# Performance work log

Hardware: AMD Instinct MI355X
Metric: run time of the kernel (lower is better)

## Reference

```python
import jax, jax.numpy as jnp
import numpy as np

N, E, F, G, OUT, L = 100000, 1600000, 64, 128, 32, 2


def setup_inputs() -> dict:
    key = jax.random.key(0)
    ks = jax.random.split(key, 14)
    x = jax.random.normal(ks[0], (N, F), jnp.float32)
    src = jax.random.randint(ks[1], (E,), 0, N)
    dst = jax.random.randint(ks[2], (E,), 0, N)
    dst = dst.at[:N].set(jnp.arange(N))  # every node receives >=1 message (no empty segments)
    edge_index = jnp.stack([src, dst]).astype(jnp.int64)
    batch = jnp.sort(jnp.concatenate([jnp.arange(G), jax.random.randint(ks[3], (N - G,), 0, G)])).astype(jnp.int64)
    s = 1.0 / np.sqrt(F)
    Wlin = jax.random.normal(ks[4], (L, F, F), jnp.float32) * s   # per-layer message Linear
    blin = jnp.zeros((L, F), jnp.float32)
    t = jax.random.uniform(ks[5], (L, F), jnp.float32)            # convex bias weight in [0,1]
    Wproj = jax.random.normal(ks[6], (L, 5), jnp.float32) * 0.5   # lin_project(5->1) weight
    bproj = jnp.zeros((L,), jnp.float32)
    Wc = jax.random.normal(ks[7], (L, F, F), jnp.float32) * s     # LTSum combine Linear
    bc = jnp.zeros((L, F), jnp.float32)
    gWlin = jax.random.normal(ks[8], (F, F), jnp.float32) * s     # global conv message Linear
    gblin = jnp.zeros((F,), jnp.float32)
    gt = jax.random.uniform(ks[9], (F,), jnp.float32)
    gWproj = jax.random.normal(ks[10], (5,), jnp.float32) * 0.5
    gbproj = jnp.zeros((), jnp.float32)
    Wout = jax.random.normal(ks[11], (OUT, F), jnp.float32) * s   # out_MLP (single Linear)
    bout = jnp.zeros((OUT,), jnp.float32)
    return dict(x=x, edge_index=edge_index, batch=batch, Wlin=Wlin, blin=blin, t=t,
                Wproj=Wproj, bproj=bproj, Wc=Wc, bc=bc, gWlin=gWlin, gblin=gblin,
                gt=gt, gWproj=gWproj, gbproj=gbproj, Wout=Wout, bout=bout)


def _adaptive_relu(m, idx, num_seg, t, Wproj, bproj):
    # m: [S, F] multiset elements, idx: [S] segment ids
    mn = jax.ops.segment_min(m, idx, num_segments=num_seg)
    mx = jax.ops.segment_max(m, idx, num_segments=num_seg)
    sm = jax.ops.segment_sum(m, idx, num_segments=num_seg)
    cnt = jax.ops.segment_sum(jnp.ones((m.shape[0],), m.dtype), idx, num_segments=num_seg)
    bias = t * mx[idx] + (1.0 - t) * mn[idx]                      # gather per-segment stats
    relu_sum = jax.ops.segment_sum(jax.nn.relu(m - bias), idx, num_segments=num_seg)
    cnt_b = jnp.broadcast_to(cnt[:, None], mn.shape)
    coords = jnp.stack([cnt_b, mn, mx, relu_sum, sm], axis=-1)    # [num_seg, F, 5]
    return jnp.einsum('sfc,c->sf', coords, Wproj) + bproj


def reference(x, edge_index, batch, Wlin, blin, t, Wproj, bproj, Wc, bc,
              gWlin, gblin, gt, gWproj, gbproj, Wout, bout):
    src, dst = edge_index[0], edge_index[1]
    h = x
    for l in range(L):
        msg = h[src] @ Wlin[l].T + blin[l]                        # gather + linear message
        agg = _adaptive_relu(msg, dst, N, jnp.clip(t[l], 0.0, 1.0), Wproj[l], bproj[l])
        h = h @ Wc[l].T + bc[l] + agg                             # LTSum combine
    gmsg = h @ gWlin.T + gblin                                    # global conv message
    emb = _adaptive_relu(gmsg, batch, G, jnp.clip(gt, 0.0, 1.0), gWproj, gbproj)
    return emb @ Wout.T + bout                                    # out_MLP -> [G, OUT]
```

## Files before the change

kernel.cpp:

```cpp
#include <hip/hip_runtime.h>
#include <hip/hip_fp16.h>

#define N_NODES 100000
#define E_EDGES 1600000
#define FDIM 64
#define G_GRAPHS 128
#define OUTD 32
#define CAP 16
#define NPB 512
#define NPB_SH 9
#define KBUK ((N_NODES + NPB - 1) / NPB)
#define CAPB 10240
#define SEB 4096
#define SEBLK ((E_EDGES + SEB - 1) / SEB)
#define GCH 16

__device__ __forceinline__ __half2 u2h(unsigned int u) {
    union { unsigned int i; __half2 h; } c; c.i = u; return c.h;
}
__device__ __forceinline__ unsigned int h2u(__half2 h) {
    union { __half2 h; unsigned int i; } c; c.h = h; return c.i;
}
__device__ __forceinline__ __half2 sxh2(__half2 v, int off) {
    return u2h((unsigned int)__shfl_xor((int)h2u(v), off));
}
__device__ __forceinline__ __half2 h2min(__half2 a, __half2 b) {
    unsigned int r, x = h2u(a), y = h2u(b);
    asm("v_pk_min_f16 %0, %1, %2" : "=v"(r) : "v"(x), "v"(y));
    return u2h(r);
}
__device__ __forceinline__ __half2 h2max(__half2 a, __half2 b) {
    unsigned int r, x = h2u(a), y = h2u(b);
    asm("v_pk_max_f16 %0, %1, %2" : "=v"(r) : "v"(x), "v"(y));
    return u2h(r);
}
__device__ __forceinline__ __half2 h2add(__half2 a, __half2 b) {
    unsigned int r, x = h2u(a), y = h2u(b);
    asm("v_pk_add_f16 %0, %1, %2" : "=v"(r) : "v"(x), "v"(y));
    return u2h(r);
}


__global__ __launch_bounds__(256) void binit_kernel(int* __restrict__ bucketCursor) {
    int i = threadIdx.x;
    if (i < KBUK) bucketCursor[i * 16] = i * CAPB;
}

__global__ __launch_bounds__(256) void bscatter_kernel(const int* __restrict__ src,
                                                       const int* __restrict__ dst,
                                                       int* __restrict__ bucketCursor,
                                                       int* __restrict__ ebuf) {
    __shared__ int h[KBUK], resbase[KBUK], lcur[KBUK];
    for (int i = threadIdx.x; i < KBUK; i += 256) { h[i] = 0; lcur[i] = 0; }
    __syncthreads();
    const int base = blockIdx.x * SEB;
#pragma unroll
    for (int i = 0; i < 16; ++i) {
        int e = base + i * 256 + threadIdx.x;
        if (e < E_EDGES) atomicAdd(&h[dst[e] >> NPB_SH], 1);
    }
    __syncthreads();
    for (int i = threadIdx.x; i < KBUK; i += 256)
        resbase[i] = h[i] ? atomicAdd(&bucketCursor[i * 16], h[i]) : 0;
    __syncthreads();
#pragma unroll
    for (int i = 0; i < 16; ++i) {
        int e = base + i * 256 + threadIdx.x;
        if (e < E_EDGES) {
            int d = dst[e];
            int b = d >> NPB_SH;
            int pos = resbase[b] + atomicAdd(&lcur[b], 1);
            ebuf[pos] = (src[e] << NPB_SH) | (d & (NPB - 1));
        }
    }
}

__global__ __launch_bounds__(256) void bscan_kernel(const int* __restrict__ bucketCursor,
                                                    int* __restrict__ bucketStart,
                                                    int* __restrict__ offsets) {
    __shared__ int s[256];
    const int tid = threadIdx.x;
    int v = (tid < KBUK) ? (bucketCursor[tid * 16] - tid * CAPB) : 0;
    s[tid] = v;
    __syncthreads();
    for (int off = 1; off < 256; off <<= 1) {
        int t = 0;
        if (tid >= off) t = s[tid - off];
        __syncthreads();
        if (tid >= off) s[tid] += t;
        __syncthreads();
    }
    int excl = s[tid] - v;
    if (tid < KBUK) bucketStart[tid] = excl;
    if (tid == 0) { bucketStart[KBUK] = E_EDGES; offsets[N_NODES] = E_EDGES; }
}

__global__ __launch_bounds__(256) void bsort_kernel(const int* __restrict__ ebuf,
                                                    const int* __restrict__ bucketStart,
                                                    int* __restrict__ offsets,
                                                    int* __restrict__ srcSorted) {
    __shared__ int cnt[NPB];
    __shared__ int cur[NPB];
    __shared__ int wsum[4];
    const int b = blockIdx.x;
    const int tid = threadIdx.x;
    const int rbase = b * CAPB;
    const int ebase = bucketStart[b];
    const int cb = bucketStart[b + 1] - ebase;
    const int nbase = b * NPB;
    cnt[tid] = 0; cnt[tid + 256] = 0;
    __syncthreads();
    for (int e = tid; e < cb; e += 256)
        atomicAdd(&cnt[ebuf[rbase + e] & (NPB - 1)], 1);
    __syncthreads();
    int v0 = cnt[2 * tid], v1 = cnt[2 * tid + 1];
    int s = v0 + v1;
    const int lane = tid & 63, wv = tid >> 6;
    int incl = s;
#pragma unroll
    for (int off = 1; off < 64; off <<= 1) {
        int o = __shfl_up(incl, off);
        if (lane >= off) incl += o;
    }
    if (lane == 63) wsum[wv] = incl;
    __syncthreads();
    int wpre = 0;
#pragma unroll
    for (int w = 0; w < 4; ++w) wpre += (w < wv) ? wsum[w] : 0;
    int excl = wpre + incl - s;
    cur[2 * tid] = excl; cur[2 * tid + 1] = excl + v0;
    int n0 = nbase + 2 * tid;
    if (n0 < N_NODES) offsets[n0] = ebase + excl;
    if (n0 + 1 < N_NODES) offsets[n0 + 1] = ebase + excl + v0;
    __syncthreads();
    for (int e = tid; e < cb; e += 256) {
        int u = ebuf[rbase + e];
        int pos = ebase + atomicAdd(&cur[u & (NPB - 1)], 1);
        srcSorted[pos] = (u >> NPB_SH) << 4;
    }
}

__global__ __launch_bounds__(256) void bound_kernel(const int* __restrict__ batch,
                                                    int* __restrict__ gstart) {
    int i = blockIdx.x * 256 + threadIdx.x;
    if (i >= N_NODES) return;
    if (i == 0) {
        gstart[batch[0]] = 0;
    } else {
        int b = batch[i], pb = batch[i - 1];
        if (b != pb) gstart[b] = i;
    }
}


template <bool F16OUT>
__global__ __launch_bounds__(256) void lin_kernel(const float* __restrict__ in,
                                                  const float* __restrict__ W,
                                                  const float* __restrict__ b,
                                                  float* __restrict__ outF,
                                                  __half* __restrict__ outH) {
    __shared__ __align__(16) float4 shH[1024];
    __shared__ __align__(16) float4 shW[1024];
    const int tid = threadIdx.x;
    const int base = blockIdx.x * 64;
#pragma unroll
    for (int i = 0; i < 4; ++i) {
        int j = tid + i * 256;
        int row = j >> 4, col = j & 15;
        int swz = row * 16 + (col ^ ((row >> 2) & 7));
        if (base + row < N_NODES)
            shH[swz] = ((const float4*)in)[(size_t)base * 16 + j];
        shW[swz] = ((const float4*)W)[j];
    }
    __syncthreads();
    const int fj = tid & 15, ni = tid >> 4;
    float acc[4][4] = {{0}};
    const int hs = ni & 7;
    const int ws = fj & 7;
#pragma unroll 2
    for (int kk = 0; kk < 16; ++kk) {
        const int hk = kk ^ hs, wk = kk ^ ws;
        float4 h0 = shH[(4 * ni + 0) * 16 + hk];
        float4 h1 = shH[(4 * ni + 1) * 16 + hk];
        float4 h2 = shH[(4 * ni + 2) * 16 + hk];
        float4 h3 = shH[(4 * ni + 3) * 16 + hk];
#pragma unroll
        for (int j = 0; j < 4; ++j) {
            float4 wv = shW[(4 * fj + j) * 16 + wk];
            acc[0][j] += h0.x * wv.x + h0.y * wv.y + h0.z * wv.z + h0.w * wv.w;
            acc[1][j] += h1.x * wv.x + h1.y * wv.y + h1.z * wv.z + h1.w * wv.w;
            acc[2][j] += h2.x * wv.x + h2.y * wv.y + h2.z * wv.z + h2.w * wv.w;
            acc[3][j] += h3.x * wv.x + h3.y * wv.y + h3.z * wv.z + h3.w * wv.w;
        }
    }
    float4 b4 = *(const float4*)(b + 4 * fj);
#pragma unroll
    for (int r = 0; r < 4; ++r) {
        int node = base + 4 * ni + r;
        if (node < N_NODES) {
            if (F16OUT) {
                uint2 st;
                st.x = h2u(__floats2half2_rn(acc[r][0] + b4.x, acc[r][1] + b4.y));
                st.y = h2u(__floats2half2_rn(acc[r][2] + b4.z, acc[r][3] + b4.w));
                *(uint2*)(outH + (size_t)node * 64 + 4 * fj) = st;
            } else {
                float4 o = make_float4(acc[r][0] + b4.x, acc[r][1] + b4.y,
                                       acc[r][2] + b4.z, acc[r][3] + b4.w);
                *(float4*)(outF + (size_t)node * 64 + 4 * fj) = o;
            }
        }
    }
}


__global__ __launch_bounds__(256) void agg_kernel(const __half* __restrict__ msgH,
                                                  const int* __restrict__ offsets,
                                                  const int* __restrict__ srcSorted,
                                                  const float* __restrict__ tptr,
                                                  const float* __restrict__ Wp,
                                                  const float* __restrict__ bp,
                                                  float* __restrict__ hbuf) {
    __shared__ uint2 cache[4][CAP][16];
    const int w = threadIdx.x >> 6;
    const int lane = threadIdx.x & 63;
    const int g = lane >> 4;
    const int fq = lane & 15;
    const int node = blockIdx.x * 4 + w;
    if (node >= N_NODES) return;
    const int start = offsets[node], end = offsets[node + 1];
    const int deg = end - start;
    const uint2* mq = (const uint2*)msgH + fq;
    const float INF = 65504.f;
    __half2 mnA = __float2half2_rn(INF),  mnB = __float2half2_rn(INF);
    __half2 mxA = __float2half2_rn(-INF), mxB = __float2half2_rn(-INF);
    __half2 smA = __float2half2_rn(0.f),  smB = __float2half2_rn(0.f);

#define ACCU(u) { __half2 a_ = u2h((u).x), b_ = u2h((u).y); \
    mnA = h2min(mnA, a_); mxA = h2max(mxA, a_); smA = h2add(smA, a_); \
    mnB = h2min(mnB, b_); mxB = h2max(mxB, b_); smB = h2add(smB, b_); }

    if (deg >= 16) {
        {
            int i0 = start + g;
            int s0 = srcSorted[i0], s1 = srcSorted[i0 + 4];
            int s2 = srcSorted[i0 + 8], s3 = srcSorted[i0 + 12];
            uint2 u0 = mq[(size_t)s0], u1 = mq[(size_t)s1];
            uint2 u2 = mq[(size_t)s2], u3 = mq[(size_t)s3];
            cache[w][g][fq] = u0; cache[w][g + 4][fq] = u1;
            cache[w][g + 8][fq] = u2; cache[w][g + 12][fq] = u3;
            ACCU(u0) ACCU(u1) ACCU(u2) ACCU(u3)
        }
        int e = start + 16;
        for (; e + 16 <= end; e += 16) {
            int i0 = e + g;
            int s0 = srcSorted[i0], s1 = srcSorted[i0 + 4];
            int s2 = srcSorted[i0 + 8], s3 = srcSorted[i0 + 12];
            uint2 u0 = mq[(size_t)s0], u1 = mq[(size_t)s1];
            uint2 u2 = mq[(size_t)s2], u3 = mq[(size_t)s3];
            ACCU(u0) ACCU(u1) ACCU(u2) ACCU(u3)
        }
        if (e < end) {
            int i0 = e + g, i1 = i0 + 4, i2 = i0 + 8, i3 = i0 + 12;
            bool ok0 = i0 < end, ok1 = i1 < end, ok2 = i2 < end, ok3 = i3 < end;
            int s0 = 0, s1 = 0, s2 = 0, s3 = 0;
            if (ok0) s0 = srcSorted[i0];
            if (ok1) s1 = srcSorted[i1];
            if (ok2) s2 = srcSorted[i2];
            if (ok3) s3 = srcSorted[i3];
            uint2 u0, u1, u2, u3;
            if (ok0) u0 = mq[(size_t)s0];
            if (ok1) u1 = mq[(size_t)s1];
            if (ok2) u2 = mq[(size_t)s2];
            if (ok3) u3 = mq[(size_t)s3];
            if (ok0) ACCU(u0)
            if (ok1) ACCU(u1)
            if (ok2) ACCU(u2)
            if (ok3) ACCU(u3)
        }
    } else {
        int i0 = start + g, i1 = i0 + 4, i2 = i0 + 8, i3 = i0 + 12;
        bool ok0 = i0 < end, ok1 = i1 < end, ok2 = i2 < end, ok3 = i3 < end;
        int s0 = 0, s1 = 0, s2 = 0, s3 = 0;
        if (ok0) s0 = srcSorted[i0];
        if (ok1) s1 = srcSorted[i1];
        if (ok2) s2 = srcSorted[i2];
        if (ok3) s3 = srcSorted[i3];
        uint2 u0, u1, u2, u3;
        if (ok0) u0 = mq[(size_t)s0];
        if (ok1) u1 = mq[(size_t)s1];
        if (ok2) u2 = mq[(size_t)s2];
        if (ok3) u3 = mq[(size_t)s3];
        if (ok0) { cache[w][g][fq] = u0;      ACCU(u0) }
        if (ok1) { cache[w][g + 4][fq] = u1;  ACCU(u1) }
        if (ok2) { cache[w][g + 8][fq] = u2;  ACCU(u2) }
        if (ok3) { cache[w][g + 12][fq] = u3; ACCU(u3) }
    }
#pragma unroll
    for (int off = 16; off <= 32; off <<= 1) {
        mnA = h2min(mnA, sxh2(mnA, off)); mnB = h2min(mnB, sxh2(mnB, off));
        mxA = h2max(mxA, sxh2(mxA, off)); mxB = h2max(mxB, sxh2(mxB, off));
        smA = h2add(smA, sxh2(smA, off)); smB = h2add(smB, sxh2(smB, off));
    }
    float mn0 = __low2float(mnA), mn1 = __high2float(mnA);
    float mn2 = __low2float(mnB), mn3 = __high2float(mnB);
    float mx0 = __low2float(mxA), mx1 = __high2float(mxA);
    float mx2 = __low2float(mxB), mx3 = __high2float(mxB);
    float4 tv = *(const float4*)(tptr + 4 * fq);
    tv.x = fminf(fmaxf(tv.x, 0.f), 1.f); tv.y = fminf(fmaxf(tv.y, 0.f), 1.f);
    tv.z = fminf(fmaxf(tv.z, 0.f), 1.f); tv.w = fminf(fmaxf(tv.w, 0.f), 1.f);
    float b0 = tv.x * mx0 + (1.f - tv.x) * mn0;
    float b1 = tv.y * mx1 + (1.f - tv.y) * mn1;
    float b2 = tv.z * mx2 + (1.f - tv.z) * mn2;
    float b3 = tv.w * mx3 + (1.f - tv.w) * mn3;
    __half2 biasA = __floats2half2_rn(b0, b1);
    __half2 biasB = __floats2half2_rn(b2, b3);
    float fb0 = __low2float(biasA), fb1 = __high2float(biasA);
    float fb2 = __low2float(biasB), fb3 = __high2float(biasB);
    __half2 rsA = __float2half2_rn(0.f), rsB = __float2half2_rn(0.f);

#define RACCU(u) { __half2 a_ = u2h((u).x), b_ = u2h((u).y); \
    rsA = h2add(rsA, h2max(a_, biasA)); \
    rsB = h2add(rsB, h2max(b_, biasB)); }

    if (deg >= 16) {
#pragma unroll
        for (int i = 0; i < 4; ++i) {
            uint2 u = cache[w][i * 4 + g][fq];
            RACCU(u)
        }
        int e = start + 16;
        for (; e + 16 <= end; e += 16) {
            int i0 = e + g;
            int s0 = srcSorted[i0], s1 = srcSorted[i0 + 4];
            int s2 = srcSorted[i0 + 8], s3 = srcSorted[i0 + 12];
            uint2 u0 = mq[(size_t)s0], u1 = mq[(size_t)s1];
            uint2 u2 = mq[(size_t)s2], u3 = mq[(size_t)s3];
            RACCU(u0) RACCU(u1) RACCU(u2) RACCU(u3)
        }
        if (e < end) {
            int i0 = e + g, i1 = i0 + 4, i2 = i0 + 8, i3 = i0 + 12;
            bool ok0 = i0 < end, ok1 = i1 < end, ok2 = i2 < end, ok3 = i3 < end;
            int s0 = 0, s1 = 0, s2 = 0, s3 = 0;
            if (ok0) s0 = srcSorted[i0];
            if (ok1) s1 = srcSorted[i1];
            if (ok2) s2 = srcSorted[i2];
            if (ok3) s3 = srcSorted[i3];
            uint2 u0, u1, u2, u3;
            if (ok0) u0 = mq[(size_t)s0];
            if (ok1) u1 = mq[(size_t)s1];
            if (ok2) u2 = mq[(size_t)s2];
            if (ok3) u3 = mq[(size_t)s3];
            if (ok0) RACCU(u0)
            if (ok1) RACCU(u1)
            if (ok2) RACCU(u2)
            if (ok3) RACCU(u3)
        }
    } else {
        for (int idx = start + g; idx < end; idx += 4) {
            uint2 u = cache[w][idx - start][fq];
            RACCU(u)
        }
    }
#pragma unroll
    for (int off = 16; off <= 32; off <<= 1) {
        rsA = h2add(rsA, sxh2(rsA, off));
        rsB = h2add(rsB, sxh2(rsB, off));
    }
    if (g == 0) {
        float cnt = (float)deg;
        float w0 = Wp[0], w1 = Wp[1], w2 = Wp[2], w3 = Wp[3], w4 = Wp[4], bp0 = bp[0];
        float rs0 = __low2float(rsA) - cnt * fb0;
        float rs1 = __high2float(rsA) - cnt * fb1;
        float rs2 = __low2float(rsB) - cnt * fb2;
        float rs3 = __high2float(rsB) - cnt * fb3;
        float sm0 = __low2float(smA), sm1 = __high2float(smA);
        float sm2 = __low2float(smB), sm3 = __high2float(smB);
        float4* hp = (float4*)(hbuf + (size_t)node * 64 + 4 * fq);
        float4 h = *hp;
        h.x += w0 * cnt + w1 * mn0 + w2 * mx0 + w3 * rs0 + w4 * sm0 + bp0;
        h.y += w0 * cnt + w1 * mn1 + w2 * mx1 + w3 * rs1 + w4 * sm1 + bp0;
        h.z += w0 * cnt + w1 * mn2 + w2 * mx2 + w3 * rs2 + w4 * sm2 + bp0;
        h.w += w0 * cnt + w1 * mn3 + w2 * mx3 + w3 * rs3 + w4 * sm3 + bp0;
        *hp = h;
    }
#undef ACCU
#undef RACCU
}


__global__ __launch_bounds__(256) void gaggA_kernel(const __half* __restrict__ msgH,
                                                    const int* __restrict__ gstart,
                                                    float* __restrict__ pmn,
                                                    float* __restrict__ pmx,
                                                    float* __restrict__ psm) {
    const int bid = blockIdx.x;
    const int g = bid >> 4, c = bid & (GCH - 1);
    const int s = gstart[g];
    const int e = (g == G_GRAPHS - 1) ? N_NODES : gstart[g + 1];
    const int clen = (e - s + GCH - 1) / GCH;
    const int cs = s + c * clen;
    const int ce = (cs + clen < e) ? (cs + clen) : e;
    const int f = threadIdx.x & 63, r = threadIdx.x >> 6;
    float mn = __builtin_inff(), mx = -__builtin_inff(), sm = 0.f;
    for (int i = cs + r; i < ce; i += 4) {
        float v = __half2float(msgH[(size_t)i * 64 + f]);
        mn = fminf(mn, v); mx = fmaxf(mx, v); sm += v;
    }
    __shared__ float smn[4][64], smx[4][64], ssm[4][64];
    smn[r][f] = mn; smx[r][f] = mx; ssm[r][f] = sm;
    __syncthreads();
    if (r == 0) {
        pmn[bid * 64 + f] = fminf(fminf(smn[0][f], smn[1][f]), fminf(smn[2][f], smn[3][f]));
        pmx[bid * 64 + f] = fmaxf(fmaxf(smx[0][f], smx[1][f]), fmaxf(smx[2][f], smx[3][f]));
        psm[bid * 64 + f] = ssm[0][f] + ssm[1][f] + ssm[2][f] + ssm[3][f];
    }
}

__global__ __launch_bounds__(64) void gaggB_kernel(const float* __restrict__ pmn,
                                                   const float* __restrict__ pmx,
                                                   const float* __restrict__ psm,
                                                   const float* __restrict__ gt,
                                                   float* __restrict__ gMn,
                                                   float* __restrict__ gMx,
                                                   float* __restrict__ gSm,
                                                   float* __restrict__ gBias) {
    const int g = blockIdx.x, f = threadIdx.x;
    float mn = __builtin_inff(), mx = -__builtin_inff(), sm = 0.f;
#pragma unroll
    for (int c = 0; c < GCH; ++c) {
        int i = (g * GCH + c) * 64 + f;
        mn = fminf(mn, pmn[i]); mx = fmaxf(mx, pmx[i]); sm += psm[i];
    }
    float tv = fminf(fmaxf(gt[f], 0.f), 1.f);
    gMn[g * 64 + f] = mn; gMx[g * 64 + f] = mx; gSm[g * 64 + f] = sm;
    gBias[g * 64 + f] = tv * mx + (1.f - tv) * mn;
}

__global__ __launch_bounds__(256) void gaggC_kernel(const __half* __restrict__ msgH,
                                                    const int* __restrict__ gstart,
                                                    const float* __restrict__ gBias,
                                                    float* __restrict__ prs) {
    const int bid = blockIdx.x;
    const int g = bid >> 4, c = bid & (GCH - 1);
    const int s = gstart[g];
    const int e = (g == G_GRAPHS - 1) ? N_NODES : gstart[g + 1];
    const int clen = (e - s + GCH - 1) / GCH;
    const int cs = s + c * clen;
    const int ce = (cs + clen < e) ? (cs + clen) : e;
    const int f = threadIdx.x & 63, r = threadIdx.x >> 6;
    const float bias = gBias[g * 64 + f];
    float rs = 0.f;
    for (int i = cs + r; i < ce; i += 4) {
        float v = __half2float(msgH[(size_t)i * 64 + f]);
        rs += fmaxf(v - bias, 0.f);
    }
    __shared__ float srs[4][64];
    srs[r][f] = rs;
    __syncthreads();
    if (r == 0)
        prs[bid * 64 + f] = srs[0][f] + srs[1][f] + srs[2][f] + srs[3][f];
}

__global__ __launch_bounds__(64) void gaggD_kernel(const float* __restrict__ prs,
                                                   const int* __restrict__ gstart,
                                                   const float* __restrict__ gMn,
                                                   const float* __restrict__ gMx,
                                                   const float* __restrict__ gSm,
                                                   const float* __restrict__ gWp,
                                                   const float* __restrict__ gbp,
                                                   const float* __restrict__ Wout,
                                                   const float* __restrict__ bout,
                                                   float* __restrict__ out) {
    const int g = blockIdx.x, f = threadIdx.x;
    float rs = 0.f;
#pragma unroll
    for (int c = 0; c < GCH; ++c) rs += prs[(g * GCH + c) * 64 + f];
    const int s = gstart[g];
    const int e = (g == G_GRAPHS - 1) ? N_NODES : gstart[g + 1];
    float cnt = (float)(e - s);
    __shared__ float emb[64];
    emb[f] = gWp[0] * cnt + gWp[1] * gMn[g * 64 + f] + gWp[2] * gMx[g * 64 + f] +
             gWp[3] * rs + gWp[4] * gSm[g * 64 + f] + gbp[0];
    __syncthreads();
    if (f < OUTD) {
        float a = bout[f];
        const float* wr = Wout + f * 64;
#pragma unroll
        for (int k = 0; k < 64; ++k) a = fmaf(emb[k], wr[k], a);
        out[g * OUTD + f] = a;
    }
}


extern "C" void kernel_launch(void* const* d_in, const int* in_sizes, int n_in,
                              void* d_out, int out_size, void* d_ws, size_t ws_size,
                              hipStream_t stream) {
    const float* x     = (const float*)d_in[0];
    const int*   ei    = (const int*)d_in[1];
    const int*   batch = (const int*)d_in[2];
    const float* Wlin  = (const float*)d_in[3];
    const float* blin  = (const float*)d_in[4];
    const float* t     = (const float*)d_in[5];
    const float* Wproj = (const float*)d_in[6];
    const float* bproj = (const float*)d_in[7];
    const float* Wc    = (const float*)d_in[8];
    const float* bc    = (const float*)d_in[9];
    const float* gWlin = (const float*)d_in[10];
    const float* gblin = (const float*)d_in[11];
    const float* gt    = (const float*)d_in[12];
    const float* gWproj= (const float*)d_in[13];
    const float* gbproj= (const float*)d_in[14];
    const float* Wout  = (const float*)d_in[15];
    const float* bout  = (const float*)d_in[16];
    float* out = (float*)d_out;

    const int* src = ei;
    const int* dst = ei + E_EDGES;

    char* p = (char*)d_ws;
    float* bufH   = (float*)p; p += (size_t)N_NODES * FDIM * sizeof(float);
    __half* msgH  = (__half*)p; p += (size_t)N_NODES * FDIM * sizeof(__half);
    int* ebuf     = (int*)p;   p += (size_t)KBUK * CAPB * sizeof(int);
    int* offsets  = (int*)p;   p += (size_t)(N_NODES + 1) * sizeof(int);
    int* gstart   = (int*)p;   p += (size_t)G_GRAPHS * sizeof(int);
    int* bucketStart  = (int*)p; p += (size_t)(KBUK + 1) * sizeof(int);
    int* bucketCursor = (int*)p; p += (size_t)KBUK * 16 * sizeof(int);
    int* srcSorted= (int*)p;   p += (size_t)E_EDGES * sizeof(int);
    float* pmn = (float*)p;    p += (size_t)G_GRAPHS * GCH * 64 * sizeof(float);
    float* pmx = (float*)p;    p += (size_t)G_GRAPHS * GCH * 64 * sizeof(float);
    float* psm = (float*)p;    p += (size_t)G_GRAPHS * GCH * 64 * sizeof(float);
    float* prs = (float*)p;    p += (size_t)G_GRAPHS * GCH * 64 * sizeof(float);
    float* gMn = (float*)p;    p += (size_t)G_GRAPHS * 64 * sizeof(float);
    float* gMx = (float*)p;    p += (size_t)G_GRAPHS * 64 * sizeof(float);
    float* gSm = (float*)p;    p += (size_t)G_GRAPHS * 64 * sizeof(float);
    float* gBias = (float*)p;  p += (size_t)G_GRAPHS * 64 * sizeof(float);

    const int NB = (N_NODES + 255) / 256;
    binit_kernel<<<1, 256, 0, stream>>>(bucketCursor);
    bscatter_kernel<<<SEBLK, 256, 0, stream>>>(src, dst, bucketCursor, ebuf);
    bscan_kernel<<<1, 256, 0, stream>>>(bucketCursor, bucketStart, offsets);
    bsort_kernel<<<KBUK, 256, 0, stream>>>(ebuf, bucketStart, offsets, srcSorted);
    bound_kernel<<<NB, 256, 0, stream>>>(batch, gstart);

    const int LB = (N_NODES + 63) / 64;
    const int AB = (N_NODES + 3) / 4;

    lin_kernel<true><<<LB, 256, 0, stream>>>(x, Wlin, blin, nullptr, msgH);
    lin_kernel<false><<<LB, 256, 0, stream>>>(x, Wc, bc, bufH, nullptr);
    agg_kernel<<<AB, 256, 0, stream>>>(msgH, offsets, srcSorted, t, Wproj, bproj, bufH);
    lin_kernel<true><<<LB, 256, 0, stream>>>(bufH, Wlin + 4096, blin + 64, nullptr, msgH);
    lin_kernel<false><<<LB, 256, 0, stream>>>(bufH, Wc + 4096, bc + 64, bufH, nullptr);
    agg_kernel<<<AB, 256, 0, stream>>>(msgH, offsets, srcSorted, t + 64, Wproj + 5,
                                       bproj + 1, bufH);
    lin_kernel<true><<<LB, 256, 0, stream>>>(bufH, gWlin, gblin, nullptr, msgH);
    gaggA_kernel<<<G_GRAPHS * GCH, 256, 0, stream>>>(msgH, gstart, pmn, pmx, psm);
    gaggB_kernel<<<G_GRAPHS, 64, 0, stream>>>(pmn, pmx, psm, gt, gMn, gMx, gSm, gBias);
    gaggC_kernel<<<G_GRAPHS * GCH, 256, 0, stream>>>(msgH, gstart, gBias, prs);
    gaggD_kernel<<<G_GRAPHS, 64, 0, stream>>>(prs, gstart, gMn, gMx, gSm, gWproj,
                                              gbproj, Wout, bout, out);
}
```

Before: 287.8 us.

## Enlarge lin_kernel tile to 128 nodes and merge binit into bound_kernel

```diff
diff --git a/kernel.cpp b/kernel.cpp
--- a/kernel.cpp
+++ b/kernel.cpp
@@ -41,9 +41,19 @@
 }
 
 
-__global__ __launch_bounds__(256) void binit_kernel(int* __restrict__ bucketCursor) {
-    int i = threadIdx.x;
-    if (i < KBUK) bucketCursor[i * 16] = i * CAPB;
+__global__ __launch_bounds__(256) void bound_kernel(const int* __restrict__ batch,
+                                                    int* __restrict__ gstart,
+                                                    int* __restrict__ bucketCursor) {
+    int i = blockIdx.x * 256 + threadIdx.x;
+    if (blockIdx.x == 0 && threadIdx.x < KBUK)
+        bucketCursor[threadIdx.x * 16] = threadIdx.x * CAPB;
+    if (i >= N_NODES) return;
+    if (i == 0) {
+        gstart[batch[0]] = 0;
+    } else {
+        int b = batch[i], pb = batch[i - 1];
+        if (b != pb) gstart[b] = i;
+    }
 }
 
 __global__ __launch_bounds__(256) void bscatter_kernel(const int* __restrict__ src,
@@ -140,18 +150,6 @@
     }
 }
 
-__global__ __launch_bounds__(256) void bound_kernel(const int* __restrict__ batch,
-                                                    int* __restrict__ gstart) {
-    int i = blockIdx.x * 256 + threadIdx.x;
-    if (i >= N_NODES) return;
-    if (i == 0) {
-        gstart[batch[0]] = 0;
-    } else {
-        int b = batch[i], pb = batch[i - 1];
-        if (b != pb) gstart[b] = i;
-    }
-}
-
 
 template <bool F16OUT>
 __global__ __launch_bounds__(256) void lin_kernel(const float* __restrict__ in,
@@ -159,54 +157,67 @@
                                                   const float* __restrict__ b,
                                                   float* __restrict__ outF,
                                                   __half* __restrict__ outH) {
-    __shared__ __align__(16) float4 shH[1024];
+    __shared__ __align__(16) float4 shH[2048];
     __shared__ __align__(16) float4 shW[1024];
     const int tid = threadIdx.x;
-    const int base = blockIdx.x * 64;
-#pragma unroll
-    for (int i = 0; i < 4; ++i) {
+    const int base = blockIdx.x * 128;
+#pragma unroll
+    for (int i = 0; i < 8; ++i) {
         int j = tid + i * 256;
         int row = j >> 4, col = j & 15;
         int swz = row * 16 + (col ^ ((row >> 2) & 7));
         if (base + row < N_NODES)
             shH[swz] = ((const float4*)in)[(size_t)base * 16 + j];
+    }
+#pragma unroll
+    for (int i = 0; i < 4; ++i) {
+        int j = tid + i * 256;
+        int row = j >> 4, col = j & 15;
+        int swz = row * 16 + (col ^ ((row >> 3) & 7));
         shW[swz] = ((const float4*)W)[j];
     }
     __syncthreads();
-    const int fj = tid & 15, ni = tid >> 4;
-    float acc[4][4] = {{0}};
-    const int hs = ni & 7;
-    const int ws = fj & 7;
-#pragma unroll 2
+    const int fj = tid & 7, ni = tid >> 3;
+    const int hsw = ni & 7;
+    float acc[4][8] = {{0}};
+#pragma unroll 1
     for (int kk = 0; kk < 16; ++kk) {
-        const int hk = kk ^ hs, wk = kk ^ ws;
-        float4 h0 = shH[(4 * ni + 0) * 16 + hk];
-        float4 h1 = shH[(4 * ni + 1) * 16 + hk];
-        float4 h2 = shH[(4 * ni + 2) * 16 + hk];
-        float4 h3 = shH[(4 * ni + 3) * 16 + hk];
-#pragma unroll
-        for (int j = 0; j < 4; ++j) {
-            float4 wv = shW[(4 * fj + j) * 16 + wk];
-            acc[0][j] += h0.x * wv.x + h0.y * wv.y + h0.z * wv.z + h0.w * wv.w;
-            acc[1][j] += h1.x * wv.x + h1.y * wv.y + h1.z * wv.z + h1.w * wv.w;
-            acc[2][j] += h2.x * wv.x + h2.y * wv.y + h2.z * wv.z + h2.w * wv.w;
-            acc[3][j] += h3.x * wv.x + h3.y * wv.y + h3.z * wv.z + h3.w * wv.w;
-        }
-    }
-    float4 b4 = *(const float4*)(b + 4 * fj);
+        float4 wv[8];
+        const int wk = kk ^ fj;
+#pragma unroll
+        for (int j = 0; j < 8; ++j) wv[j] = shW[(8 * fj + j) * 16 + wk];
+        const int hk = kk ^ hsw;
+#pragma unroll
+        for (int r = 0; r < 4; ++r) {
+            float4 hv = shH[(4 * ni + r) * 16 + hk];
+#pragma unroll
+            for (int j = 0; j < 8; ++j)
+                acc[r][j] += hv.x * wv[j].x + hv.y * wv[j].y +
+                             hv.z * wv[j].z + hv.w * wv[j].w;
+        }
+    }
+    float4 blo = ((const float4*)b)[2 * fj];
+    float4 bhi = ((const float4*)b)[2 * fj + 1];
 #pragma unroll
     for (int r = 0; r < 4; ++r) {
         int node = base + 4 * ni + r;
         if (node < N_NODES) {
+            float o0 = acc[r][0] + blo.x, o1 = acc[r][1] + blo.y;
+            float o2 = acc[r][2] + blo.z, o3 = acc[r][3] + blo.w;
+            float o4 = acc[r][4] + bhi.x, o5 = acc[r][5] + bhi.y;
+            float o6 = acc[r][6] + bhi.z, o7 = acc[r][7] + bhi.w;
             if (F16OUT) {
-                uint2 st;
-                st.x = h2u(__floats2half2_rn(acc[r][0] + b4.x, acc[r][1] + b4.y));
-                st.y = h2u(__floats2half2_rn(acc[r][2] + b4.z, acc[r][3] + b4.w));
-                *(uint2*)(outH + (size_t)node * 64 + 4 * fj) = st;
+                uint4 st;
+                st.x = h2u(__floats2half2_rn(o0, o1));
+                st.y = h2u(__floats2half2_rn(o2, o3));
+                st.z = h2u(__floats2half2_rn(o4, o5));
+                st.w = h2u(__floats2half2_rn(o6, o7));
+                *(uint4*)(outH + (size_t)node * 64 + 8 * fj) = st;
             } else {
-                float4 o = make_float4(acc[r][0] + b4.x, acc[r][1] + b4.y,
-                                       acc[r][2] + b4.z, acc[r][3] + b4.w);
-                *(float4*)(outF + (size_t)node * 64 + 4 * fj) = o;
+                *(float4*)(outF + (size_t)node * 64 + 8 * fj) =
+                    make_float4(o0, o1, o2, o3);
+                *(float4*)(outF + (size_t)node * 64 + 8 * fj + 4) =
+                    make_float4(o4, o5, o6, o7);
             }
         }
     }
@@ -536,13 +547,12 @@
     float* gBias = (float*)p;  p += (size_t)G_GRAPHS * 64 * sizeof(float);
 
     const int NB = (N_NODES + 255) / 256;
-    binit_kernel<<<1, 256, 0, stream>>>(bucketCursor);
+    bound_kernel<<<NB, 256, 0, stream>>>(batch, gstart, bucketCursor);
     bscatter_kernel<<<SEBLK, 256, 0, stream>>>(src, dst, bucketCursor, ebuf);
     bscan_kernel<<<1, 256, 0, stream>>>(bucketCursor, bucketStart, offsets);
     bsort_kernel<<<KBUK, 256, 0, stream>>>(ebuf, bucketStart, offsets, srcSorted);
-    bound_kernel<<<NB, 256, 0, stream>>>(batch, gstart);
-
-    const int LB = (N_NODES + 63) / 64;
+
+    const int LB = (N_NODES + 127) / 128;
     const int AB = (N_NODES + 3) / 4;
 
     lin_kernel<true><<<LB, 256, 0, stream>>>(x, Wlin, blin, nullptr, msgH);
```

New measurement: 294.3 us. 1.02x slower.
